# Optimization experiments

Measured on AMD Instinct MI355X. Metric: run time of the kernel, lower is better.

The kernel has to match this reference:

```python
import jax, jax.numpy as jnp
import numpy as np

NUM_LAYERS = 2
INPUT_SIZE = 256
HIDDEN_SIZE = 512
OUTPUT_SIZE = 256
BATCH = 32
SEQ = 2048


def setup_inputs() -> dict:
    key = jax.random.key(0)
    ks = jax.random.split(key, 12)
    s = 1.0 / np.sqrt(HIDDEN_SIZE)
    H4 = 4 * HIDDEN_SIZE
    x = jax.random.normal(ks[0], (BATCH, SEQ, INPUT_SIZE), dtype=jnp.float32)
    # layer 0: input_size -> hidden; layer 1: hidden -> hidden (torch gate order i,f,g,o)
    w_ih0 = jax.random.uniform(ks[1], (H4, INPUT_SIZE), minval=-s, maxval=s)
    w_hh0 = jax.random.uniform(ks[2], (H4, HIDDEN_SIZE), minval=-s, maxval=s)
    b0 = jax.random.uniform(ks[3], (H4,), minval=-s, maxval=s)  # b_ih0 + b_hh0 combined
    w_ih1 = jax.random.uniform(ks[4], (H4, HIDDEN_SIZE), minval=-s, maxval=s)
    w_hh1 = jax.random.uniform(ks[5], (H4, HIDDEN_SIZE), minval=-s, maxval=s)
    b1 = jax.random.uniform(ks[6], (H4,), minval=-s, maxval=s)
    w_fc = jax.random.uniform(ks[7], (OUTPUT_SIZE, HIDDEN_SIZE), minval=-s, maxval=s)
    b_fc = jax.random.uniform(ks[8], (OUTPUT_SIZE,), minval=-s, maxval=s)
    return {"x": x, "w_ih0": w_ih0, "w_hh0": w_hh0, "b0": b0,
            "w_ih1": w_ih1, "w_hh1": w_hh1, "b1": b1,
            "w_fc": w_fc, "b_fc": b_fc}


def _lstm_layer(x, w_ih, w_hh, b):
    # x: [B, T, In] -> output hidden sequence [B, T, H]
    B = x.shape[0]
    H = w_hh.shape[1]
    # precompute all input projections: [T, B, 4H]
    xg = (jnp.einsum('bti,gi->btg', x, w_ih) + b).transpose(1, 0, 2)

    def step(carry, xg_t):
        h, c = carry
        gates = xg_t + h @ w_hh.T  # [B, 4H]
        i, f, g, o = jnp.split(gates, 4, axis=-1)
        i = jax.nn.sigmoid(i)
        f = jax.nn.sigmoid(f)
        g = jnp.tanh(g)
        o = jax.nn.sigmoid(o)
        c = f * c + i * g
        h = o * jnp.tanh(c)
        return (h, c), h

    h0 = jnp.zeros((B, H), dtype=x.dtype)
    c0 = jnp.zeros((B, H), dtype=x.dtype)
    _, hs = jax.lax.scan(step, (h0, c0), xg)  # hs: [T, B, H]
    return hs.transpose(1, 0, 2)


def reference(x, w_ih0, w_hh0, b0, w_ih1, w_hh1, b1, w_fc, b_fc):
    h = _lstm_layer(x, w_ih0, w_hh0, b0)
    h = _lstm_layer(h, w_ih1, w_hh1, b1)
    return jnp.einsum('bth,oh->bto', h, w_fc) + b_fc
```

## Files before the change

### kernel.cpp

```cpp
#include <hip/hip_runtime.h>

typedef __attribute__((ext_vector_type(8))) short bf16x8;
typedef __attribute__((ext_vector_type(4))) float f32x4;
typedef __attribute__((ext_vector_type(4))) unsigned int u32x4;

#define T_SEQ 2048
#define RING  64
#define NL0   32
#define NL1   32
#define NFC   8
#define NWG   (NL0 + NL1 + NFC)
#define SLOT_STRIDE 16

#define HSWZ(o) ((o) ^ ((((o) >> 10) & 7) << 4))

static __device__ __forceinline__ unsigned short f2b(float f) {
  unsigned u = __float_as_uint(f);
  u = (u + 0x7fffu + ((u >> 16) & 1u)) >> 16;
  return (unsigned short)u;
}
static __device__ __forceinline__ float sigm(float x) { return 1.f / (1.f + __expf(-x)); }
static __device__ __forceinline__ float tanh_f(float x) { return 2.f / (1.f + __expf(-2.f * x)) - 1.f; }

static __device__ __forceinline__ u32x4 llc_load16(const void* p) {
  u32x4 v;
  asm volatile("global_load_dwordx4 %0, %1, off sc0 sc1" : "=v"(v) : "v"(p) : "memory");
  return v;
}
static __device__ __forceinline__ void llc_store4(void* p, unsigned v) {
  asm volatile("global_store_dword %0, %1, off sc0 sc1" :: "v"(p), "v"(v) : "memory");
}
static __device__ __forceinline__ void vmwait() {
  asm volatile("s_waitcnt vmcnt(0)" ::: "memory");
}

static __device__ __forceinline__ int flag_ld(const int* p) {
  return __hip_atomic_load(p, __ATOMIC_RELAXED, __HIP_MEMORY_SCOPE_SYSTEM);
}
static __device__ __forceinline__ void flag_st(int* p, int v) {
  __hip_atomic_store(p, v, __ATOMIC_RELAXED, __HIP_MEMORY_SCOPE_SYSTEM);
}

static __device__ __forceinline__ void poll_flags(const int* s0, const int* s1, const int* sf,
                                                  int n0, int n1, int nf) {
  if (threadIdx.x < 64) {
    const int lane = threadIdx.x;
    const int* p1 = (lane < 32) ? (s0 + lane * SLOT_STRIDE) : (s1 + (lane - 32) * SLOT_STRIDE);
    const int* p2 = sf + (lane & 7) * SLOT_STRIDE;
    const int need1 = (lane < 32) ? n0 : n1;
    const bool chk2 = (lane < 8);
    for (;;) {
      int v1 = flag_ld(p1);
      int v2 = flag_ld(p2);
      int ok = (v1 >= need1) && (!chk2 || (v2 >= nf));
      if (__all(ok)) break;
    }
  }
  __syncthreads();
}

__global__ void lstm_prologue(
    const float* __restrict__ x, const float* __restrict__ wih0, const float* __restrict__ whh0,
    const float* __restrict__ wih1, const float* __restrict__ whh1, const float* __restrict__ wfc,
    unsigned short* __restrict__ wl0, unsigned short* __restrict__ wl1,
    unsigned short* __restrict__ wfcp, unsigned short* __restrict__ xb,
    unsigned short* __restrict__ h0r, unsigned short* __restrict__ h1r,
    int* __restrict__ flags) {
  size_t tid = (size_t)blockIdx.x * blockDim.x + threadIdx.x;
  size_t nthr = (size_t)gridDim.x * blockDim.x;
  for (size_t i = tid; i < (size_t)2048 * 768; i += nthr) {
    int r = (int)(i / 768), k = (int)(i % 768);
    float v = (k < 256) ? wih0[(size_t)r * 256 + k] : whh0[(size_t)r * 512 + (k - 256)];
    wl0[i] = f2b(v);
  }
  for (size_t i = tid; i < (size_t)2048 * 1024; i += nthr) {
    int r = (int)(i >> 10), k = (int)(i & 1023);
    float v = (k < 512) ? wih1[((size_t)r << 9) + k] : whh1[((size_t)r << 9) + (k - 512)];
    wl1[i] = f2b(v);
  }
  for (size_t i = tid; i < 131072; i += nthr) wfcp[i] = f2b(wfc[i]);
  for (size_t i = tid; i < (size_t)16777216; i += nthr) {
    int ii = (int)(i & 255), b = (int)((i >> 8) & 31), t = (int)(i >> 13);
    xb[i] = f2b(x[((size_t)b * 2048 + t) * 256 + ii]);
  }
  for (size_t i = tid; i < (NL0 + NL1 + NFC) * SLOT_STRIDE; i += nthr) flags[i] = 0;
  for (size_t i = tid; i < 32 * 512; i += nthr) {
    h0r[(size_t)(RING - 1) * 32 * 512 + i] = 0;
    h1r[(size_t)(RING - 1) * 32 * 512 + i] = 0;
  }
}

template <int ISL0>
static __device__ void lstm_path(
    const unsigned short* __restrict__ xb, const unsigned short* __restrict__ wl,
    const float* __restrict__ bias,
    unsigned short* __restrict__ h0r, unsigned short* __restrict__ h1r,
    int* s0, int* s1, int* sf, int wid2,
    unsigned short* hA, unsigned short* xA, float (*gates)[32][18]) {
  const int tid = threadIdx.x;
  const int wave = tid >> 6, lane = tid & 63, l15 = lane & 15, kgrp = lane >> 4;
  const int u0 = wid2 * 16;
  constexpr int K = ISL0 ? 768 : 1024;
  constexpr int NKW = ISL0 ? 24 : 32;
  const unsigned short* wrow = wl + (size_t)(wave * 512 + u0 + l15) * K;

  bf16x8 wf[NKW];
#pragma unroll
  for (int kk = 0; kk < NKW; ++kk) wf[kk] = *(const bf16x8*)(wrow + kk * 32 + kgrp * 8);

  const int ue = 2 * (tid & 7);
  const int be = tid >> 3;
  const float bi0 = bias[0 * 512 + u0 + ue], bi1 = bias[0 * 512 + u0 + ue + 1];
  const float bf0 = bias[1 * 512 + u0 + ue], bf1 = bias[1 * 512 + u0 + ue + 1];
  const float bg0 = bias[2 * 512 + u0 + ue], bg1 = bias[2 * 512 + u0 + ue + 1];
  const float bo0 = bias[3 * 512 + u0 + ue], bo1 = bias[3 * 512 + u0 + ue + 1];
  float cc0 = 0.f, cc1 = 0.f;
  unsigned short* myring = ISL0 ? h0r : h1r;
  int* myslot = (ISL0 ? s0 : s1) + wid2 * SLOT_STRIDE;

  for (int t = 0; t < T_SEQ; ++t) {
    bf16x8 xf0[8], xf1[8];
    if (ISL0) {
      const unsigned short* xt = xb + (size_t)t * (32 * 256);
#pragma unroll
      for (int kk = 0; kk < 8; ++kk) {
        xf0[kk] = *(const bf16x8*)(xt + l15 * 256 + kk * 32 + kgrp * 8);
        xf1[kk] = *(const bf16x8*)(xt + (16 + l15) * 256 + kk * 32 + kgrp * 8);
      }
    }

    if (ISL0) {
      poll_flags(s0, s1, sf, t, t - (RING - 1), -1000000);
    } else {
      poll_flags(s0, s1, sf, t + 1, t, t - (RING - 1));
    }

    const unsigned short* hprev = myring + (size_t)((t - 1) & (RING - 1)) * (32 * 512);
    u32x4 th[8], tx[8];
#pragma unroll
    for (int k = 0; k < 8; ++k)
      th[k] = llc_load16((const char*)hprev + (size_t)(tid + k * 256) * 16);
    if (!ISL0) {
      const unsigned short* h0cur = h0r + (size_t)(t & (RING - 1)) * (32 * 512);
#pragma unroll
      for (int k = 0; k < 8; ++k)
        tx[k] = llc_load16((const char*)h0cur + (size_t)(tid + k * 256) * 16);
    }
    vmwait();
#pragma unroll
    for (int k = 0; k < 8; ++k) {
      int off = (tid + k * 256) * 16;
      *(u32x4*)((char*)hA + HSWZ(off)) = th[k];
    }
    if (!ISL0) {
#pragma unroll
      for (int k = 0; k < 8; ++k) {
        int off = (tid + k * 256) * 16;
        *(u32x4*)((char*)xA + HSWZ(off)) = tx[k];
      }
    }
    __syncthreads();

    f32x4 acc0 = {0.f, 0.f, 0.f, 0.f}, acc1 = {0.f, 0.f, 0.f, 0.f};
    if (ISL0) {
#pragma unroll
      for (int kk = 0; kk < 8; ++kk) {
        acc0 = __builtin_amdgcn_mfma_f32_16x16x32_bf16(xf0[kk], wf[kk], acc0, 0, 0, 0);
        acc1 = __builtin_amdgcn_mfma_f32_16x16x32_bf16(xf1[kk], wf[kk], acc1, 0, 0, 0);
      }
#pragma unroll
      for (int kk = 0; kk < 16; ++kk) {
        int cb = (kk * 32 + kgrp * 8) * 2;
        bf16x8 a0 = *(const bf16x8*)((const char*)hA + HSWZ(l15 * 1024 + cb));
        bf16x8 a1 = *(const bf16x8*)((const char*)hA + HSWZ((16 + l15) * 1024 + cb));
        acc0 = __builtin_amdgcn_mfma_f32_16x16x32_bf16(a0, wf[8 + kk], acc0, 0, 0, 0);
        acc1 = __builtin_amdgcn_mfma_f32_16x16x32_bf16(a1, wf[8 + kk], acc1, 0, 0, 0);
      }
    } else {
#pragma unroll
      for (int kk = 0; kk < 16; ++kk) {
        int cb = (kk * 32 + kgrp * 8) * 2;
        bf16x8 a0 = *(const bf16x8*)((const char*)xA + HSWZ(l15 * 1024 + cb));
        bf16x8 a1 = *(const bf16x8*)((const char*)xA + HSWZ((16 + l15) * 1024 + cb));
        acc0 = __builtin_amdgcn_mfma_f32_16x16x32_bf16(a0, wf[kk], acc0, 0, 0, 0);
        acc1 = __builtin_amdgcn_mfma_f32_16x16x32_bf16(a1, wf[kk], acc1, 0, 0, 0);
      }
#pragma unroll
      for (int kk = 0; kk < 16; ++kk) {
        int cb = (kk * 32 + kgrp * 8) * 2;
        bf16x8 a0 = *(const bf16x8*)((const char*)hA + HSWZ(l15 * 1024 + cb));
        bf16x8 a1 = *(const bf16x8*)((const char*)hA + HSWZ((16 + l15) * 1024 + cb));
        acc0 = __builtin_amdgcn_mfma_f32_16x16x32_bf16(a0, wf[16 + kk], acc0, 0, 0, 0);
        acc1 = __builtin_amdgcn_mfma_f32_16x16x32_bf16(a1, wf[16 + kk], acc1, 0, 0, 0);
      }
    }
#pragma unroll
    for (int j = 0; j < 4; ++j) {
      gates[wave][kgrp * 4 + j][l15] = acc0[j];
      gates[wave][16 + kgrp * 4 + j][l15] = acc1[j];
    }
    __syncthreads();

    unsigned short* hdst = myring + (size_t)(t & (RING - 1)) * (32 * 512);
    float i0 = sigm(gates[0][be][ue] + bi0);
    float ff0 = sigm(gates[1][be][ue] + bf0);
    float g0 = tanh_f(gates[2][be][ue] + bg0);
    float o0 = sigm(gates[3][be][ue] + bo0);
    cc0 = ff0 * cc0 + i0 * g0;
    float hv0 = o0 * tanh_f(cc0);
    float i1 = sigm(gates[0][be][ue + 1] + bi1);
    float ff1 = sigm(gates[1][be][ue + 1] + bf1);
    float g1 = tanh_f(gates[2][be][ue + 1] + bg1);
    float o1 = sigm(gates[3][be][ue + 1] + bo1);
    cc1 = ff1 * cc1 + i1 * g1;
    float hv1 = o1 * tanh_f(cc1);
    unsigned pv = (unsigned)f2b(hv0) | ((unsigned)f2b(hv1) << 16);
    llc_store4(hdst + (size_t)be * 512 + u0 + ue, pv);
    vmwait();
    __syncthreads();
    if (tid == 0) flag_st(myslot, t + 1);
  }
}

__global__ void __launch_bounds__(256) lstm_main(
    const unsigned short* __restrict__ xb,
    const unsigned short* __restrict__ wl0,
    const unsigned short* __restrict__ wl1,
    const unsigned short* __restrict__ wfcp,
    const float* __restrict__ b0,
    const float* __restrict__ b1,
    const float* __restrict__ bfc,
    unsigned short* __restrict__ h0r,
    unsigned short* __restrict__ h1r,
    int* flags,
    float* __restrict__ out) {
  __shared__ __align__(16) unsigned short hA[32 * 512];
  __shared__ __align__(16) unsigned short xA[32 * 512];
  __shared__ __align__(16) float gates[4][32][18];
  const int tid = threadIdx.x;
  const int wave = tid >> 6, lane = tid & 63, l15 = lane & 15, kgrp = lane >> 4;
  const int wid = blockIdx.x;
  int* s0 = flags;
  int* s1 = flags + NL0 * SLOT_STRIDE;
  int* sf = flags + (NL0 + NL1) * SLOT_STRIDE;

  if (wid < NL0) {
    lstm_path<1>(xb, wl0, b0, h0r, h1r, s0, s1, sf, wid, hA, xA, gates);
  } else if (wid < NL0 + NL1) {
    lstm_path<0>(xb, wl1, b1, h0r, h1r, s0, s1, sf, wid - NL0, hA, xA, gates);
  } else {
    const int fcw = wid - NL0 - NL1;
    const int mt = wave >> 1, ntile = wave & 1;
    const int orow = fcw * 32 + ntile * 16 + l15;
    bf16x8 wff[16];
#pragma unroll
    for (int kk = 0; kk < 16; ++kk)
      wff[kk] = *(const bf16x8*)(wfcp + (size_t)orow * 512 + kk * 32 + kgrp * 8);
    const float bb = bfc[orow];
    for (int t = 0; t < T_SEQ; ++t) {
      poll_flags(s0, s1, sf, -1000000, t + 1, -1000000);
      const unsigned short* hcur = h1r + (size_t)(t & (RING - 1)) * (32 * 512);
      u32x4 th[8];
#pragma unroll
      for (int k = 0; k < 8; ++k)
        th[k] = llc_load16((const char*)hcur + (size_t)(tid + k * 256) * 16);
      vmwait();
#pragma unroll
      for (int k = 0; k < 8; ++k) {
        int off = (tid + k * 256) * 16;
        *(u32x4*)((char*)hA + HSWZ(off)) = th[k];
      }
      __syncthreads();
      if (tid == 0) flag_st(sf + fcw * SLOT_STRIDE, t + 1);
      f32x4 acc = {0.f, 0.f, 0.f, 0.f};
#pragma unroll
      for (int kk = 0; kk < 16; ++kk) {
        int row = mt * 16 + l15;
        bf16x8 a = *(const bf16x8*)((const char*)hA + HSWZ(row * 1024 + (kk * 32 + kgrp * 8) * 2));
        acc = __builtin_amdgcn_mfma_f32_16x16x32_bf16(a, wff[kk], acc, 0, 0, 0);
      }
#pragma unroll
      for (int j = 0; j < 4; ++j) {
        int b = mt * 16 + kgrp * 4 + j;
        out[((size_t)b * T_SEQ + t) * 256 + orow] = acc[j] + bb;
      }
    }
  }
}

extern "C" void kernel_launch(void* const* d_in, const int* in_sizes, int n_in,
                              void* d_out, int out_size, void* d_ws, size_t ws_size,
                              hipStream_t stream) {
  const float* x    = (const float*)d_in[0];
  const float* wih0 = (const float*)d_in[1];
  const float* whh0 = (const float*)d_in[2];
  const float* b0   = (const float*)d_in[3];
  const float* wih1 = (const float*)d_in[4];
  const float* whh1 = (const float*)d_in[5];
  const float* b1   = (const float*)d_in[6];
  const float* wfc  = (const float*)d_in[7];
  const float* bfc  = (const float*)d_in[8];
  float* outp = (float*)d_out;

  char* ws = (char*)d_ws;
  size_t off = 0;
  unsigned short* wl0p = (unsigned short*)(ws + off); off += (size_t)2048 * 768 * 2;
  unsigned short* wl1p = (unsigned short*)(ws + off); off += (size_t)2048 * 1024 * 2;
  unsigned short* wfcp = (unsigned short*)(ws + off); off += (size_t)256 * 512 * 2;
  unsigned short* xbp  = (unsigned short*)(ws + off); off += (size_t)2048 * 32 * 256 * 2;
  unsigned short* h0rp = (unsigned short*)(ws + off); off += (size_t)RING * 32 * 512 * 2;
  unsigned short* h1rp = (unsigned short*)(ws + off); off += (size_t)RING * 32 * 512 * 2;
  int* flagsp = (int*)(ws + off); off += (size_t)NWG * SLOT_STRIDE * sizeof(int);

  lstm_prologue<<<dim3(1024), dim3(256), 0, stream>>>(
      x, wih0, whh0, wih1, whh1, wfc, wl0p, wl1p, wfcp, xbp, h0rp, h1rp, flagsp);

  lstm_main<<<dim3(NWG), dim3(256), 0, stream>>>(
      xbp, wl0p, wl1p, wfcp, b0, b1, bfc, h0rp, h1rp, flagsp, outp);
}
```

Measured before the change: 8.449 ms.

## Replace per-step flag polling with tagged ring data and coarse backpressure

Each hidden-state element is stored as a 32-bit word carrying a timestep tag in its upper half. Consumers spin on the ring data until the tags match, which removes the per-step flag store, the vmwait and the barrier on the producer side, and the flag poll on the consumer side. Backpressure flags are now published only every four steps, and the ring is shrunk to 16 slots. The changes double ring traffic and add retry loops on partially written data. They also depend on the coarse guard distance matching the smaller ring, which is a correctness risk.

```diff
diff --git a/kernel.cpp b/kernel.cpp
--- a/kernel.cpp
+++ b/kernel.cpp
@@ -3,14 +3,17 @@
 typedef __attribute__((ext_vector_type(8))) short bf16x8;
 typedef __attribute__((ext_vector_type(4))) float f32x4;
 typedef __attribute__((ext_vector_type(4))) unsigned int u32x4;
+typedef __attribute__((ext_vector_type(2))) unsigned int u32x2;
 
 #define T_SEQ 2048
-#define RING  64
+#define RING  16
 #define NL0   32
 #define NL1   32
 #define NFC   8
 #define NWG   (NL0 + NL1 + NFC)
 #define SLOT_STRIDE 16
+#define SLOT_U32 (32 * 512)
+#define TAGW(t) ((unsigned)((t) + 1) << 16)
 
 #define HSWZ(o) ((o) ^ ((((o) >> 10) & 7) << 4))
 
@@ -27,13 +30,12 @@
   asm volatile("global_load_dwordx4 %0, %1, off sc0 sc1" : "=v"(v) : "v"(p) : "memory");
   return v;
 }
-static __device__ __forceinline__ void llc_store4(void* p, unsigned v) {
-  asm volatile("global_store_dword %0, %1, off sc0 sc1" :: "v"(p), "v"(v) : "memory");
+static __device__ __forceinline__ void llc_store8(void* p, u32x2 v) {
+  asm volatile("global_store_dwordx2 %0, %1, off sc0 sc1" :: "v"(p), "v"(v) : "memory");
 }
 static __device__ __forceinline__ void vmwait() {
   asm volatile("s_waitcnt vmcnt(0)" ::: "memory");
 }
-
 static __device__ __forceinline__ int flag_ld(const int* p) {
   return __hip_atomic_load(p, __ATOMIC_RELAXED, __HIP_MEMORY_SCOPE_SYSTEM);
 }
@@ -41,22 +43,51 @@
   __hip_atomic_store(p, v, __ATOMIC_RELAXED, __HIP_MEMORY_SCOPE_SYSTEM);
 }
 
-static __device__ __forceinline__ void poll_flags(const int* s0, const int* s1, const int* sf,
-                                                  int n0, int n1, int nf) {
-  if (threadIdx.x < 64) {
-    const int lane = threadIdx.x;
-    const int* p1 = (lane < 32) ? (s0 + lane * SLOT_STRIDE) : (s1 + (lane - 32) * SLOT_STRIDE);
-    const int* p2 = sf + (lane & 7) * SLOT_STRIDE;
-    const int need1 = (lane < 32) ? n0 : n1;
-    const bool chk2 = (lane < 8);
-    for (;;) {
-      int v1 = flag_ld(p1);
-      int v2 = flag_ld(p2);
-      int ok = (v1 >= need1) && (!chk2 || (v2 >= nf));
-      if (__all(ok)) break;
-    }
-  }
-  __syncthreads();
+template <int NC>
+static __device__ __forceinline__ void guard_poll(const int* prog, int need) {
+  const int lane = threadIdx.x & 63;
+  for (;;) {
+    int v = 0x7fffffff;
+    if (lane < NC) v = flag_ld(prog + lane * SLOT_STRIDE);
+    if (__all(v >= need)) break;
+  }
+}
+
+template <int TWO>
+static __device__ void stage_rings(const unsigned* srcA, unsigned tagA, unsigned short* dstA,
+                                   const unsigned* srcB, unsigned tagB, unsigned short* dstB,
+                                   int tid) {
+  constexpr int NCH = TWO ? 32 : 16;
+  u32x4 v[NCH];
+  unsigned mask = TWO ? 0xffffffffu : 0xffffu;
+  while (mask) {
+#pragma unroll
+    for (int k = 0; k < NCH; ++k)
+      if ((mask >> k) & 1u) {
+        const unsigned* s = (k < 16) ? srcA : srcB;
+        v[k] = llc_load16((const char*)s + ((size_t)tid + (k & 15) * 256) * 16);
+      }
+    vmwait();
+    unsigned nm = 0;
+#pragma unroll
+    for (int k = 0; k < NCH; ++k)
+      if ((mask >> k) & 1u) {
+        unsigned tw = (k < 16) ? tagA : tagB;
+        unsigned d = ((v[k].x ^ tw) | (v[k].y ^ tw) | (v[k].z ^ tw) | (v[k].w ^ tw)) & 0xffff0000u;
+        if (d == 0) {
+          int c = tid + (k & 15) * 256;
+          u32x2 p;
+          p.x = (v[k].x & 0xffffu) | (v[k].y << 16);
+          p.y = (v[k].z & 0xffffu) | (v[k].w << 16);
+          int off = (c >> 7) * 1024 + (c & 127) * 8;
+          unsigned short* dst = (k < 16) ? dstA : dstB;
+          *(u32x2*)((char*)dst + HSWZ(off)) = p;
+        } else {
+          nm |= 1u << k;
+        }
+      }
+    mask = nm;
+  }
 }
 
 __global__ void lstm_prologue(
@@ -64,7 +95,7 @@
     const float* __restrict__ wih1, const float* __restrict__ whh1, const float* __restrict__ wfc,
     unsigned short* __restrict__ wl0, unsigned short* __restrict__ wl1,
     unsigned short* __restrict__ wfcp, unsigned short* __restrict__ xb,
-    unsigned short* __restrict__ h0r, unsigned short* __restrict__ h1r,
+    unsigned* __restrict__ h0r, unsigned* __restrict__ h1r,
     int* __restrict__ flags) {
   size_t tid = (size_t)blockIdx.x * blockDim.x + threadIdx.x;
   size_t nthr = (size_t)gridDim.x * blockDim.x;
@@ -83,10 +114,10 @@
     int ii = (int)(i & 255), b = (int)((i >> 8) & 31), t = (int)(i >> 13);
     xb[i] = f2b(x[((size_t)b * 2048 + t) * 256 + ii]);
   }
-  for (size_t i = tid; i < (NL0 + NL1 + NFC) * SLOT_STRIDE; i += nthr) flags[i] = 0;
-  for (size_t i = tid; i < 32 * 512; i += nthr) {
-    h0r[(size_t)(RING - 1) * 32 * 512 + i] = 0;
-    h1r[(size_t)(RING - 1) * 32 * 512 + i] = 0;
+  for (size_t i = tid; i < (NL0 + NFC) * SLOT_STRIDE; i += nthr) flags[i] = 0;
+  for (size_t i = tid; i < SLOT_U32; i += nthr) {
+    h0r[(size_t)(RING - 1) * SLOT_U32 + i] = 0;
+    h1r[(size_t)(RING - 1) * SLOT_U32 + i] = 0;
   }
 }
 
@@ -94,8 +125,8 @@
 static __device__ void lstm_path(
     const unsigned short* __restrict__ xb, const unsigned short* __restrict__ wl,
     const float* __restrict__ bias,
-    unsigned short* __restrict__ h0r, unsigned short* __restrict__ h1r,
-    int* s0, int* s1, int* sf, int wid2,
+    unsigned* __restrict__ h0r, unsigned* __restrict__ h1r,
+    int* s1prog, int* sfprog, int wid2,
     unsigned short* hA, unsigned short* xA, float (*gates)[32][18]) {
   const int tid = threadIdx.x;
   const int wave = tid >> 6, lane = tid & 63, l15 = lane & 15, kgrp = lane >> 4;
@@ -115,10 +146,14 @@
   const float bg0 = bias[2 * 512 + u0 + ue], bg1 = bias[2 * 512 + u0 + ue + 1];
   const float bo0 = bias[3 * 512 + u0 + ue], bo1 = bias[3 * 512 + u0 + ue + 1];
   float cc0 = 0.f, cc1 = 0.f;
-  unsigned short* myring = ISL0 ? h0r : h1r;
-  int* myslot = (ISL0 ? s0 : s1) + wid2 * SLOT_STRIDE;
+  unsigned* myring = ISL0 ? h0r : h1r;
 
   for (int t = 0; t < T_SEQ; ++t) {
+    if ((t & 3) == 0 && t >= 16 && wave == 0) {
+      if (ISL0) guard_poll<NL1>(s1prog, t - 8);
+      else      guard_poll<NFC>(sfprog, t - 8);
+    }
+
     bf16x8 xf0[8], xf1[8];
     if (ISL0) {
       const unsigned short* xt = xb + (size_t)t * (32 * 256);
@@ -130,36 +165,12 @@
     }
 
     if (ISL0) {
-      poll_flags(s0, s1, sf, t, t - (RING - 1), -1000000);
+      stage_rings<0>(myring + (size_t)((t - 1) & (RING - 1)) * SLOT_U32, TAGW(t - 1), hA,
+                     nullptr, 0, nullptr, tid);
     } else {
-      poll_flags(s0, s1, sf, t + 1, t, t - (RING - 1));
-    }
-
-    const unsigned short* hprev = myring + (size_t)((t - 1) & (RING - 1)) * (32 * 512);
-    u32x4 th[8], tx[8];
-#pragma unroll
-    for (int k = 0; k < 8; ++k)
-      th[k] = llc_load16((const char*)hprev + (size_t)(tid + k * 256) * 16);
-    if (!ISL0) {
-      const unsigned short* h0cur = h0r + (size_t)(t & (RING - 1)) * (32 * 512);
-#pragma unroll
-      for (int k = 0; k < 8; ++k)
-        tx[k] = llc_load16((const char*)h0cur + (size_t)(tid + k * 256) * 16);
-    }
-    vmwait();
-#pragma unroll
-    for (int k = 0; k < 8; ++k) {
-      int off = (tid + k * 256) * 16;
-      *(u32x4*)((char*)hA + HSWZ(off)) = th[k];
-    }
-    if (!ISL0) {
-#pragma unroll
-      for (int k = 0; k < 8; ++k) {
-        int off = (tid + k * 256) * 16;
-        *(u32x4*)((char*)xA + HSWZ(off)) = tx[k];
-      }
-    }
-    __syncthreads();
+      stage_rings<1>(h1r + (size_t)((t - 1) & (RING - 1)) * SLOT_U32, TAGW(t - 1), hA,
+                     h0r + (size_t)(t & (RING - 1)) * SLOT_U32, TAGW(t), xA, tid);
+    }
 
     f32x4 acc0 = {0.f, 0.f, 0.f, 0.f}, acc1 = {0.f, 0.f, 0.f, 0.f};
     if (ISL0) {
@@ -168,6 +179,10 @@
         acc0 = __builtin_amdgcn_mfma_f32_16x16x32_bf16(xf0[kk], wf[kk], acc0, 0, 0, 0);
         acc1 = __builtin_amdgcn_mfma_f32_16x16x32_bf16(xf1[kk], wf[kk], acc1, 0, 0, 0);
       }
+    }
+    __syncthreads();
+
+    if (ISL0) {
 #pragma unroll
       for (int kk = 0; kk < 16; ++kk) {
         int cb = (kk * 32 + kgrp * 8) * 2;
@@ -201,7 +216,6 @@
     }
     __syncthreads();
 
-    unsigned short* hdst = myring + (size_t)(t & (RING - 1)) * (32 * 512);
     float i0 = sigm(gates[0][be][ue] + bi0);
     float ff0 = sigm(gates[1][be][ue] + bf0);
     float g0 = tanh_f(gates[2][be][ue] + bg0);
@@ -214,15 +228,17 @@
     float o1 = sigm(gates[3][be][ue + 1] + bo1);
     cc1 = ff1 * cc1 + i1 * g1;
     float hv1 = o1 * tanh_f(cc1);
-    unsigned pv = (unsigned)f2b(hv0) | ((unsigned)f2b(hv1) << 16);
-    llc_store4(hdst + (size_t)be * 512 + u0 + ue, pv);
-    vmwait();
-    __syncthreads();
-    if (tid == 0) flag_st(myslot, t + 1);
-  }
-}
-
-__global__ void __launch_bounds__(256) lstm_main(
+    unsigned tg = TAGW(t);
+    u32x2 pv;
+    pv.x = tg | (unsigned)f2b(hv0);
+    pv.y = tg | (unsigned)f2b(hv1);
+    llc_store8(myring + (size_t)(t & (RING - 1)) * SLOT_U32 + (size_t)be * 512 + u0 + ue, pv);
+
+    if (!ISL0 && (t & 3) == 3 && tid == 0) flag_st(s1prog + wid2 * SLOT_STRIDE, t + 1);
+  }
+}
+
+__global__ void __launch_bounds__(256, 1) lstm_main(
     const unsigned short* __restrict__ xb,
     const unsigned short* __restrict__ wl0,
     const unsigned short* __restrict__ wl1,
@@ -230,8 +246,8 @@
     const float* __restrict__ b0,
     const float* __restrict__ b1,
     const float* __restrict__ bfc,
-    unsigned short* __restrict__ h0r,
-    unsigned short* __restrict__ h1r,
+    unsigned* __restrict__ h0r,
+    unsigned* __restrict__ h1r,
     int* flags,
     float* __restrict__ out) {
   __shared__ __align__(16) unsigned short hA[32 * 512];
@@ -240,14 +256,13 @@
   const int tid = threadIdx.x;
   const int wave = tid >> 6, lane = tid & 63, l15 = lane & 15, kgrp = lane >> 4;
   const int wid = blockIdx.x;
-  int* s0 = flags;
-  int* s1 = flags + NL0 * SLOT_STRIDE;
-  int* sf = flags + (NL0 + NL1) * SLOT_STRIDE;
+  int* s1prog = flags;
+  int* sfprog = flags + NL0 * SLOT_STRIDE;
 
   if (wid < NL0) {
-    lstm_path<1>(xb, wl0, b0, h0r, h1r, s0, s1, sf, wid, hA, xA, gates);
+    lstm_path<1>(xb, wl0, b0, h0r, h1r, s1prog, sfprog, wid, hA, xA, gates);
   } else if (wid < NL0 + NL1) {
-    lstm_path<0>(xb, wl1, b1, h0r, h1r, s0, s1, sf, wid - NL0, hA, xA, gates);
+    lstm_path<0>(xb, wl1, b1, h0r, h1r, s1prog, sfprog, wid - NL0, hA, xA, gates);
   } else {
     const int fcw = wid - NL0 - NL1;
     const int mt = wave >> 1, ntile = wave & 1;
@@ -258,25 +273,15 @@
       wff[kk] = *(const bf16x8*)(wfcp + (size_t)orow * 512 + kk * 32 + kgrp * 8);
     const float bb = bfc[orow];
     for (int t = 0; t < T_SEQ; ++t) {
-      poll_flags(s0, s1, sf, -1000000, t + 1, -1000000);
-      const unsigned short* hcur = h1r + (size_t)(t & (RING - 1)) * (32 * 512);
-      u32x4 th[8];
-#pragma unroll
-      for (int k = 0; k < 8; ++k)
-        th[k] = llc_load16((const char*)hcur + (size_t)(tid + k * 256) * 16);
-      vmwait();
-#pragma unroll
-      for (int k = 0; k < 8; ++k) {
-        int off = (tid + k * 256) * 16;
-        *(u32x4*)((char*)hA + HSWZ(off)) = th[k];
-      }
+      unsigned short* buf = (t & 1) ? xA : hA;
+      stage_rings<0>(h1r + (size_t)(t & (RING - 1)) * SLOT_U32, TAGW(t), buf,
+                     nullptr, 0, nullptr, tid);
       __syncthreads();
-      if (tid == 0) flag_st(sf + fcw * SLOT_STRIDE, t + 1);
       f32x4 acc = {0.f, 0.f, 0.f, 0.f};
 #pragma unroll
       for (int kk = 0; kk < 16; ++kk) {
         int row = mt * 16 + l15;
-        bf16x8 a = *(const bf16x8*)((const char*)hA + HSWZ(row * 1024 + (kk * 32 + kgrp * 8) * 2));
+        bf16x8 a = *(const bf16x8*)((const char*)buf + HSWZ(row * 1024 + (kk * 32 + kgrp * 8) * 2));
         acc = __builtin_amdgcn_mfma_f32_16x16x32_bf16(a, wff[kk], acc, 0, 0, 0);
       }
 #pragma unroll
@@ -284,6 +289,7 @@
         int b = mt * 16 + kgrp * 4 + j;
         out[((size_t)b * T_SEQ + t) * 256 + orow] = acc[j] + bb;
       }
+      if ((t & 3) == 3 && tid == 0) flag_st(sfprog + fcw * SLOT_STRIDE, t + 1);
     }
   }
 }
@@ -308,9 +314,9 @@
   unsigned short* wl1p = (unsigned short*)(ws + off); off += (size_t)2048 * 1024 * 2;
   unsigned short* wfcp = (unsigned short*)(ws + off); off += (size_t)256 * 512 * 2;
   unsigned short* xbp  = (unsigned short*)(ws + off); off += (size_t)2048 * 32 * 256 * 2;
-  unsigned short* h0rp = (unsigned short*)(ws + off); off += (size_t)RING * 32 * 512 * 2;
-  unsigned short* h1rp = (unsigned short*)(ws + off); off += (size_t)RING * 32 * 512 * 2;
-  int* flagsp = (int*)(ws + off); off += (size_t)NWG * SLOT_STRIDE * sizeof(int);
+  unsigned* h0rp = (unsigned*)(ws + off); off += (size_t)RING * SLOT_U32 * 4;
+  unsigned* h1rp = (unsigned*)(ws + off); off += (size_t)RING * SLOT_U32 * 4;
+  int* flagsp = (int*)(ws + off); off += (size_t)(NL0 + NFC) * SLOT_STRIDE * sizeof(int);
 
   lstm_prologue<<<dim3(1024), dim3(256), 0, stream>>>(
       x, wih0, whh0, wih1, whh1, wfc, wl0p, wl1p, wfcp, xbp, h0rp, h1rp, flagsp);
```

After: 14.10 ms. 1.67x slower.

## Split recurrent matmul across waves by K, reduce gate partials in LDS

Applied to the files above, without the earlier changes.

Previously each wave computed one full gate over the whole K dimension. Now each wave covers a K-slice for all four gates and writes partial sums to a larger shared buffer, which the epilogue reduces. Each A fragment read from LDS is reused across four MFMAs, and the layer-0 input projection is issued before the wait on the h-state loads so it overlaps them. The cost is four times more LDS traffic for partials plus a reduction step. The change also sets launch bounds to one block, pins weight registers, and adds a barrier at the end of each FC step.

```diff
diff --git a/kernel.cpp b/kernel.cpp
--- a/kernel.cpp
+++ b/kernel.cpp
@@ -33,7 +33,6 @@
 static __device__ __forceinline__ void vmwait() {
   asm volatile("s_waitcnt vmcnt(0)" ::: "memory");
 }
-
 static __device__ __forceinline__ int flag_ld(const int* p) {
   return __hip_atomic_load(p, __ATOMIC_RELAXED, __HIP_MEMORY_SCOPE_SYSTEM);
 }
@@ -96,17 +95,38 @@
     const float* __restrict__ bias,
     unsigned short* __restrict__ h0r, unsigned short* __restrict__ h1r,
     int* s0, int* s1, int* sf, int wid2,
-    unsigned short* hA, unsigned short* xA, float (*gates)[32][18]) {
+    unsigned short* hA, unsigned short* xA, float (*part)[4][32][18]) {
   const int tid = threadIdx.x;
   const int wave = tid >> 6, lane = tid & 63, l15 = lane & 15, kgrp = lane >> 4;
   const int u0 = wid2 * 16;
   constexpr int K = ISL0 ? 768 : 1024;
   constexpr int NKW = ISL0 ? 24 : 32;
-  const unsigned short* wrow = wl + (size_t)(wave * 512 + u0 + l15) * K;
 
   bf16x8 wf[NKW];
-#pragma unroll
-  for (int kk = 0; kk < NKW; ++kk) wf[kk] = *(const bf16x8*)(wrow + kk * 32 + kgrp * 8);
+  if (ISL0) {
+#pragma unroll
+    for (int kk = 0; kk < 8; ++kk) {
+      wf[kk] = *(const bf16x8*)(wl + (size_t)(wave * 512 + u0 + l15) * K + kk * 32 + kgrp * 8);
+      asm volatile("" : "+v"(wf[kk]));
+    }
+#pragma unroll
+    for (int g = 0; g < 4; ++g)
+#pragma unroll
+      for (int kk = 0; kk < 4; ++kk) {
+        wf[8 + g * 4 + kk] = *(const bf16x8*)(wl + (size_t)(g * 512 + u0 + l15) * K + 256 +
+                                              wave * 128 + kk * 32 + kgrp * 8);
+        asm volatile("" : "+v"(wf[8 + g * 4 + kk]));
+      }
+  } else {
+#pragma unroll
+    for (int g = 0; g < 4; ++g)
+#pragma unroll
+      for (int kk = 0; kk < 8; ++kk) {
+        wf[g * 8 + kk] = *(const bf16x8*)(wl + (size_t)(g * 512 + u0 + l15) * K +
+                                          wave * 256 + kk * 32 + kgrp * 8);
+        asm volatile("" : "+v"(wf[g * 8 + kk]));
+      }
+  }
 
   const int ue = 2 * (tid & 7);
   const int be = tid >> 3;
@@ -146,6 +166,16 @@
       for (int k = 0; k < 8; ++k)
         tx[k] = llc_load16((const char*)h0cur + (size_t)(tid + k * 256) * 16);
     }
+
+    f32x4 px0 = {0.f, 0.f, 0.f, 0.f}, px1 = {0.f, 0.f, 0.f, 0.f};
+    if (ISL0) {
+#pragma unroll
+      for (int kk = 0; kk < 8; ++kk) {
+        px0 = __builtin_amdgcn_mfma_f32_16x16x32_bf16(xf0[kk], wf[kk], px0, 0, 0, 0);
+        px1 = __builtin_amdgcn_mfma_f32_16x16x32_bf16(xf1[kk], wf[kk], px1, 0, 0, 0);
+      }
+    }
+
     vmwait();
 #pragma unroll
     for (int k = 0; k < 8; ++k) {
@@ -161,57 +191,73 @@
     }
     __syncthreads();
 
-    f32x4 acc0 = {0.f, 0.f, 0.f, 0.f}, acc1 = {0.f, 0.f, 0.f, 0.f};
+    f32x4 acc[4][2];
+#pragma unroll
+    for (int g = 0; g < 4; ++g) {
+      acc[g][0] = f32x4{0.f, 0.f, 0.f, 0.f};
+      acc[g][1] = f32x4{0.f, 0.f, 0.f, 0.f};
+    }
     if (ISL0) {
 #pragma unroll
-      for (int kk = 0; kk < 8; ++kk) {
-        acc0 = __builtin_amdgcn_mfma_f32_16x16x32_bf16(xf0[kk], wf[kk], acc0, 0, 0, 0);
-        acc1 = __builtin_amdgcn_mfma_f32_16x16x32_bf16(xf1[kk], wf[kk], acc1, 0, 0, 0);
-      }
-#pragma unroll
-      for (int kk = 0; kk < 16; ++kk) {
-        int cb = (kk * 32 + kgrp * 8) * 2;
+      for (int kk = 0; kk < 4; ++kk) {
+        int cb = (wave * 128 + kk * 32 + kgrp * 8) * 2;
         bf16x8 a0 = *(const bf16x8*)((const char*)hA + HSWZ(l15 * 1024 + cb));
         bf16x8 a1 = *(const bf16x8*)((const char*)hA + HSWZ((16 + l15) * 1024 + cb));
-        acc0 = __builtin_amdgcn_mfma_f32_16x16x32_bf16(a0, wf[8 + kk], acc0, 0, 0, 0);
-        acc1 = __builtin_amdgcn_mfma_f32_16x16x32_bf16(a1, wf[8 + kk], acc1, 0, 0, 0);
+#pragma unroll
+        for (int g = 0; g < 4; ++g) {
+          acc[g][0] = __builtin_amdgcn_mfma_f32_16x16x32_bf16(a0, wf[8 + g * 4 + kk], acc[g][0], 0, 0, 0);
+          acc[g][1] = __builtin_amdgcn_mfma_f32_16x16x32_bf16(a1, wf[8 + g * 4 + kk], acc[g][1], 0, 0, 0);
+        }
       }
     } else {
-#pragma unroll
-      for (int kk = 0; kk < 16; ++kk) {
-        int cb = (kk * 32 + kgrp * 8) * 2;
-        bf16x8 a0 = *(const bf16x8*)((const char*)xA + HSWZ(l15 * 1024 + cb));
-        bf16x8 a1 = *(const bf16x8*)((const char*)xA + HSWZ((16 + l15) * 1024 + cb));
-        acc0 = __builtin_amdgcn_mfma_f32_16x16x32_bf16(a0, wf[kk], acc0, 0, 0, 0);
-        acc1 = __builtin_amdgcn_mfma_f32_16x16x32_bf16(a1, wf[kk], acc1, 0, 0, 0);
-      }
-#pragma unroll
-      for (int kk = 0; kk < 16; ++kk) {
-        int cb = (kk * 32 + kgrp * 8) * 2;
-        bf16x8 a0 = *(const bf16x8*)((const char*)hA + HSWZ(l15 * 1024 + cb));
-        bf16x8 a1 = *(const bf16x8*)((const char*)hA + HSWZ((16 + l15) * 1024 + cb));
-        acc0 = __builtin_amdgcn_mfma_f32_16x16x32_bf16(a0, wf[16 + kk], acc0, 0, 0, 0);
-        acc1 = __builtin_amdgcn_mfma_f32_16x16x32_bf16(a1, wf[16 + kk], acc1, 0, 0, 0);
-      }
-    }
-#pragma unroll
-    for (int j = 0; j < 4; ++j) {
-      gates[wave][kgrp * 4 + j][l15] = acc0[j];
-      gates[wave][16 + kgrp * 4 + j][l15] = acc1[j];
+      const unsigned short* Abuf = (wave < 2) ? xA : hA;
+      const int klocal0 = (wave & 1) * 256;
+#pragma unroll
+      for (int kk = 0; kk < 8; ++kk) {
+        int cb = (klocal0 + kk * 32 + kgrp * 8) * 2;
+        bf16x8 a0 = *(const bf16x8*)((const char*)Abuf + HSWZ(l15 * 1024 + cb));
+        bf16x8 a1 = *(const bf16x8*)((const char*)Abuf + HSWZ((16 + l15) * 1024 + cb));
+#pragma unroll
+        for (int g = 0; g < 4; ++g) {
+          acc[g][0] = __builtin_amdgcn_mfma_f32_16x16x32_bf16(a0, wf[g * 8 + kk], acc[g][0], 0, 0, 0);
+          acc[g][1] = __builtin_amdgcn_mfma_f32_16x16x32_bf16(a1, wf[g * 8 + kk], acc[g][1], 0, 0, 0);
+        }
+      }
+    }
+#pragma unroll
+    for (int g = 0; g < 4; ++g) {
+      f32x4 v0 = acc[g][0], v1 = acc[g][1];
+      if (ISL0 && g == wave) { v0 += px0; v1 += px1; }
+#pragma unroll
+      for (int j = 0; j < 4; ++j) {
+        part[wave][g][kgrp * 4 + j][l15] = v0[j];
+        part[wave][g][16 + kgrp * 4 + j][l15] = v1[j];
+      }
     }
     __syncthreads();
 
+    float gs0[4], gs1[4];
+#pragma unroll
+    for (int g = 0; g < 4; ++g) {
+      float a = 0.f, b = 0.f;
+#pragma unroll
+      for (int w = 0; w < 4; ++w) {
+        float2 p = *(const float2*)&part[w][g][be][ue];
+        a += p.x; b += p.y;
+      }
+      gs0[g] = a; gs1[g] = b;
+    }
     unsigned short* hdst = myring + (size_t)(t & (RING - 1)) * (32 * 512);
-    float i0 = sigm(gates[0][be][ue] + bi0);
-    float ff0 = sigm(gates[1][be][ue] + bf0);
-    float g0 = tanh_f(gates[2][be][ue] + bg0);
-    float o0 = sigm(gates[3][be][ue] + bo0);
+    float i0 = sigm(gs0[0] + bi0);
+    float ff0 = sigm(gs0[1] + bf0);
+    float g0 = tanh_f(gs0[2] + bg0);
+    float o0 = sigm(gs0[3] + bo0);
     cc0 = ff0 * cc0 + i0 * g0;
     float hv0 = o0 * tanh_f(cc0);
-    float i1 = sigm(gates[0][be][ue + 1] + bi1);
-    float ff1 = sigm(gates[1][be][ue + 1] + bf1);
-    float g1 = tanh_f(gates[2][be][ue + 1] + bg1);
-    float o1 = sigm(gates[3][be][ue + 1] + bo1);
+    float i1 = sigm(gs1[0] + bi1);
+    float ff1 = sigm(gs1[1] + bf1);
+    float g1 = tanh_f(gs1[2] + bg1);
+    float o1 = sigm(gs1[3] + bo1);
     cc1 = ff1 * cc1 + i1 * g1;
     float hv1 = o1 * tanh_f(cc1);
     unsigned pv = (unsigned)f2b(hv0) | ((unsigned)f2b(hv1) << 16);
@@ -222,7 +268,7 @@
   }
 }
 
-__global__ void __launch_bounds__(256) lstm_main(
+__global__ void __launch_bounds__(256, 1) lstm_main(
     const unsigned short* __restrict__ xb,
     const unsigned short* __restrict__ wl0,
     const unsigned short* __restrict__ wl1,
@@ -236,7 +282,7 @@
     float* __restrict__ out) {
   __shared__ __align__(16) unsigned short hA[32 * 512];
   __shared__ __align__(16) unsigned short xA[32 * 512];
-  __shared__ __align__(16) float gates[4][32][18];
+  __shared__ __align__(16) float part[4][4][32][18];
   const int tid = threadIdx.x;
   const int wave = tid >> 6, lane = tid & 63, l15 = lane & 15, kgrp = lane >> 4;
   const int wid = blockIdx.x;
@@ -245,17 +291,19 @@
   int* sf = flags + (NL0 + NL1) * SLOT_STRIDE;
 
   if (wid < NL0) {
-    lstm_path<1>(xb, wl0, b0, h0r, h1r, s0, s1, sf, wid, hA, xA, gates);
+    lstm_path<1>(xb, wl0, b0, h0r, h1r, s0, s1, sf, wid, hA, xA, part);
   } else if (wid < NL0 + NL1) {
-    lstm_path<0>(xb, wl1, b1, h0r, h1r, s0, s1, sf, wid - NL0, hA, xA, gates);
+    lstm_path<0>(xb, wl1, b1, h0r, h1r, s0, s1, sf, wid - NL0, hA, xA, part);
   } else {
     const int fcw = wid - NL0 - NL1;
     const int mt = wave >> 1, ntile = wave & 1;
     const int orow = fcw * 32 + ntile * 16 + l15;
     bf16x8 wff[16];
 #pragma unroll
-    for (int kk = 0; kk < 16; ++kk)
+    for (int kk = 0; kk < 16; ++kk) {
       wff[kk] = *(const bf16x8*)(wfcp + (size_t)orow * 512 + kk * 32 + kgrp * 8);
+      asm volatile("" : "+v"(wff[kk]));
+    }
     const float bb = bfc[orow];
     for (int t = 0; t < T_SEQ; ++t) {
       poll_flags(s0, s1, sf, -1000000, t + 1, -1000000);
@@ -284,6 +332,7 @@
         int b = mt * 16 + kgrp * 4 + j;
         out[((size_t)b * T_SEQ + t) * 256 + orow] = acc[j] + bb;
       }
+      __syncthreads();
     }
   }
 }
```

Measured after the change: 9.024 ms. 1.07x slower.

## Split LSTM step wait into staged polls overlapping input-projection MFMA with recurrent wait

Applied to the files above, without the earlier changes.

Layer-0 workgroups now issue the recurrent h loads and run the x-projection MFMAs before waiting on those loads. Layer-1 workgroups wait first only on layer-0 output, compute the input half of the gates, then wait separately on their own previous h and the FC ring slot. Flag polling skips the FC-flag loads when they are not needed. This is meant to hide sync latency on the serial recurrent path, at the cost of extra barriers and polls per step.

```diff
diff --git a/kernel.cpp b/kernel.cpp
--- a/kernel.cpp
+++ b/kernel.cpp
@@ -11,6 +11,7 @@
 #define NFC   8
 #define NWG   (NL0 + NL1 + NFC)
 #define SLOT_STRIDE 16
+#define NEG_INF (-1000000)
 
 #define HSWZ(o) ((o) ^ ((((o) >> 10) & 7) << 4))
 
@@ -33,7 +34,6 @@
 static __device__ __forceinline__ void vmwait() {
   asm volatile("s_waitcnt vmcnt(0)" ::: "memory");
 }
-
 static __device__ __forceinline__ int flag_ld(const int* p) {
   return __hip_atomic_load(p, __ATOMIC_RELAXED, __HIP_MEMORY_SCOPE_SYSTEM);
 }
@@ -41,17 +41,17 @@
   __hip_atomic_store(p, v, __ATOMIC_RELAXED, __HIP_MEMORY_SCOPE_SYSTEM);
 }
 
-static __device__ __forceinline__ void poll_flags(const int* s0, const int* s1, const int* sf,
-                                                  int n0, int n1, int nf) {
+static __device__ void spin_flags(const int* s0, int n0, const int* s1, int n1,
+                                  const int* sf, int nf) {
   if (threadIdx.x < 64) {
     const int lane = threadIdx.x;
     const int* p1 = (lane < 32) ? (s0 + lane * SLOT_STRIDE) : (s1 + (lane - 32) * SLOT_STRIDE);
+    const int need1 = (lane < 32) ? n0 : n1;
     const int* p2 = sf + (lane & 7) * SLOT_STRIDE;
-    const int need1 = (lane < 32) ? n0 : n1;
-    const bool chk2 = (lane < 8);
+    const bool chk2 = (lane < 8) && (nf > NEG_INF);
     for (;;) {
       int v1 = flag_ld(p1);
-      int v2 = flag_ld(p2);
+      int v2 = chk2 ? flag_ld(p2) : 0x7fffffff;
       int ok = (v1 >= need1) && (!chk2 || (v2 >= nf));
       if (__all(ok)) break;
     }
@@ -83,7 +83,7 @@
     int ii = (int)(i & 255), b = (int)((i >> 8) & 31), t = (int)(i >> 13);
     xb[i] = f2b(x[((size_t)b * 2048 + t) * 256 + ii]);
   }
-  for (size_t i = tid; i < (NL0 + NL1 + NFC) * SLOT_STRIDE; i += nthr) flags[i] = 0;
+  for (size_t i = tid; i < (size_t)NWG * SLOT_STRIDE; i += nthr) flags[i] = 0;
   for (size_t i = tid; i < 32 * 512; i += nthr) {
     h0r[(size_t)(RING - 1) * 32 * 512 + i] = 0;
     h1r[(size_t)(RING - 1) * 32 * 512 + i] = 0;
@@ -119,55 +119,35 @@
   int* myslot = (ISL0 ? s0 : s1) + wid2 * SLOT_STRIDE;
 
   for (int t = 0; t < T_SEQ; ++t) {
-    bf16x8 xf0[8], xf1[8];
+    f32x4 acc0 = {0.f, 0.f, 0.f, 0.f}, acc1 = {0.f, 0.f, 0.f, 0.f};
+
     if (ISL0) {
+      bf16x8 xf0[8], xf1[8];
       const unsigned short* xt = xb + (size_t)t * (32 * 256);
 #pragma unroll
       for (int kk = 0; kk < 8; ++kk) {
         xf0[kk] = *(const bf16x8*)(xt + l15 * 256 + kk * 32 + kgrp * 8);
         xf1[kk] = *(const bf16x8*)(xt + (16 + l15) * 256 + kk * 32 + kgrp * 8);
       }
-    }
-
-    if (ISL0) {
-      poll_flags(s0, s1, sf, t, t - (RING - 1), -1000000);
-    } else {
-      poll_flags(s0, s1, sf, t + 1, t, t - (RING - 1));
-    }
-
-    const unsigned short* hprev = myring + (size_t)((t - 1) & (RING - 1)) * (32 * 512);
-    u32x4 th[8], tx[8];
-#pragma unroll
-    for (int k = 0; k < 8; ++k)
-      th[k] = llc_load16((const char*)hprev + (size_t)(tid + k * 256) * 16);
-    if (!ISL0) {
-      const unsigned short* h0cur = h0r + (size_t)(t & (RING - 1)) * (32 * 512);
+      spin_flags(s0, t, s1, t - (RING - 1), sf, NEG_INF);
+
+      const unsigned short* hprev = myring + (size_t)((t - 1) & (RING - 1)) * (32 * 512);
+      u32x4 th[8];
 #pragma unroll
       for (int k = 0; k < 8; ++k)
-        tx[k] = llc_load16((const char*)h0cur + (size_t)(tid + k * 256) * 16);
-    }
-    vmwait();
-#pragma unroll
-    for (int k = 0; k < 8; ++k) {
-      int off = (tid + k * 256) * 16;
-      *(u32x4*)((char*)hA + HSWZ(off)) = th[k];
-    }
-    if (!ISL0) {
-#pragma unroll
-      for (int k = 0; k < 8; ++k) {
-        int off = (tid + k * 256) * 16;
-        *(u32x4*)((char*)xA + HSWZ(off)) = tx[k];
-      }
-    }
-    __syncthreads();
-
-    f32x4 acc0 = {0.f, 0.f, 0.f, 0.f}, acc1 = {0.f, 0.f, 0.f, 0.f};
-    if (ISL0) {
+        th[k] = llc_load16((const char*)hprev + (size_t)(tid + k * 256) * 16);
 #pragma unroll
       for (int kk = 0; kk < 8; ++kk) {
         acc0 = __builtin_amdgcn_mfma_f32_16x16x32_bf16(xf0[kk], wf[kk], acc0, 0, 0, 0);
         acc1 = __builtin_amdgcn_mfma_f32_16x16x32_bf16(xf1[kk], wf[kk], acc1, 0, 0, 0);
       }
+      vmwait();
+#pragma unroll
+      for (int k = 0; k < 8; ++k) {
+        int off = (tid + k * 256) * 16;
+        *(u32x4*)((char*)hA + HSWZ(off)) = th[k];
+      }
+      __syncthreads();
 #pragma unroll
       for (int kk = 0; kk < 16; ++kk) {
         int cb = (kk * 32 + kgrp * 8) * 2;
@@ -177,6 +157,19 @@
         acc1 = __builtin_amdgcn_mfma_f32_16x16x32_bf16(a1, wf[8 + kk], acc1, 0, 0, 0);
       }
     } else {
+      spin_flags(s0, t + 1, s1, NEG_INF, sf, NEG_INF);
+      const unsigned short* h0cur = h0r + (size_t)(t & (RING - 1)) * (32 * 512);
+      u32x4 tx[8];
+#pragma unroll
+      for (int k = 0; k < 8; ++k)
+        tx[k] = llc_load16((const char*)h0cur + (size_t)(tid + k * 256) * 16);
+      vmwait();
+#pragma unroll
+      for (int k = 0; k < 8; ++k) {
+        int off = (tid + k * 256) * 16;
+        *(u32x4*)((char*)xA + HSWZ(off)) = tx[k];
+      }
+      __syncthreads();
 #pragma unroll
       for (int kk = 0; kk < 16; ++kk) {
         int cb = (kk * 32 + kgrp * 8) * 2;
@@ -185,6 +178,20 @@
         acc0 = __builtin_amdgcn_mfma_f32_16x16x32_bf16(a0, wf[kk], acc0, 0, 0, 0);
         acc1 = __builtin_amdgcn_mfma_f32_16x16x32_bf16(a1, wf[kk], acc1, 0, 0, 0);
       }
+
+      spin_flags(s0, NEG_INF, s1, t, sf, t - (RING - 1));
+      const unsigned short* hprev = myring + (size_t)((t - 1) & (RING - 1)) * (32 * 512);
+      u32x4 th[8];
+#pragma unroll
+      for (int k = 0; k < 8; ++k)
+        th[k] = llc_load16((const char*)hprev + (size_t)(tid + k * 256) * 16);
+      vmwait();
+#pragma unroll
+      for (int k = 0; k < 8; ++k) {
+        int off = (tid + k * 256) * 16;
+        *(u32x4*)((char*)hA + HSWZ(off)) = th[k];
+      }
+      __syncthreads();
 #pragma unroll
       for (int kk = 0; kk < 16; ++kk) {
         int cb = (kk * 32 + kgrp * 8) * 2;
@@ -194,6 +201,7 @@
         acc1 = __builtin_amdgcn_mfma_f32_16x16x32_bf16(a1, wf[16 + kk], acc1, 0, 0, 0);
       }
     }
+
 #pragma unroll
     for (int j = 0; j < 4; ++j) {
       gates[wave][kgrp * 4 + j][l15] = acc0[j];
@@ -258,7 +266,7 @@
       wff[kk] = *(const bf16x8*)(wfcp + (size_t)orow * 512 + kk * 32 + kgrp * 8);
     const float bb = bfc[orow];
     for (int t = 0; t < T_SEQ; ++t) {
-      poll_flags(s0, s1, sf, -1000000, t + 1, -1000000);
+      spin_flags(s0, NEG_INF, s1, t + 1, sf, NEG_INF);
       const unsigned short* hcur = h1r + (size_t)(t & (RING - 1)) * (32 * 512);
       u32x4 th[8];
 #pragma unroll
```

Result: no change. 8.478 ms (+0.3%).
